# Performance work log

Measured on AMD Instinct MI355X. Metric: run time of the kernel, lower is better.

The kernel has to match this reference:

```python
import jax, jax.numpy as jnp
import numpy as np

HEADS = 8  # init heads


def setup_inputs() -> dict:
    key = jax.random.key(0)
    k1, k2, k3, k4 = jax.random.split(key, 4)
    B, C, L = 32, 512, 32  # batch, dim, lateral_size
    x = jax.random.normal(k1, (B, C, L, L), dtype=jnp.float32)
    # 1x1 conv with no bias == per-pixel matmul; store as [3*dim, dim]
    qkv_w = jax.random.normal(k2, (3 * C, C), dtype=jnp.float32) * (1.0 / np.sqrt(C))
    h_pos = jax.random.normal(k3, (L, 1, C), dtype=jnp.float32) * 0.02
    w_pos = jax.random.normal(k4, (1, L, C), dtype=jnp.float32) * 0.02
    return {"x": x, "qkv_w": qkv_w, "h_pos": h_pos, "w_pos": w_pos}


def reference(x, qkv_w, h_pos, w_pos):
    B, C, H, W = x.shape
    p = HEADS
    d = C // p
    n = H * W
    # QKV 1x1 conv -> [B, 3C, H, W]
    qkv = jnp.einsum('oc,bchw->bohw', qkv_w, x)
    q, k, v = jnp.split(qkv, 3, axis=1)
    # 'b (p d) h w -> b p (h w) d'
    def to_heads(t):
        return t.reshape(B, p, d, H, W).transpose(0, 1, 3, 4, 2).reshape(B, p, n, d)
    q, k, v = to_heads(q), to_heads(k), to_heads(v)
    # relative pos: [H,1,C] + [1,W,C] -> [H,W,C]; 'h w (p d) -> p (h w) d'
    rp = (h_pos + w_pos).reshape(H, W, p, d).transpose(2, 0, 1, 3).reshape(p, n, d)
    # content-position + content-content scores: [B, p, n, n]
    scores = jnp.einsum('bpnd,pmd->bpnm', q, rp) + jnp.einsum('bpnd,bpmd->bpnm', q, k)
    attn = jax.nn.softmax(scores, axis=-1)
    out = jnp.einsum('bpnm,bpmd->bpnd', attn, v)
    # 'b p (h w) d -> b (p d) h w'
    return out.reshape(B, p, H, W, d).transpose(0, 1, 4, 2, 3).reshape(B, C, H, W)
```

## Files before the change

### kernel.cpp

```cpp
#include <hip/hip_runtime.h>
#include <hip/hip_bf16.h>
#include <hip/hip_fp16.h>

#define HEADS 8
#define BB 32
#define CC 512
#define NN 1024
#define DD 64

typedef _Float16 f16;
typedef __attribute__((ext_vector_type(8))) _Float16 f16x8;
typedef __attribute__((ext_vector_type(4))) _Float16 f16x4;
typedef __attribute__((ext_vector_type(2))) __fp16 hf16x2;
typedef __attribute__((ext_vector_type(4))) float f32x4;

__device__ __forceinline__ void gload16(const f16* g, f16* l) {
    __builtin_amdgcn_global_load_lds(
        (const __attribute__((address_space(1))) void*)g,
        (__attribute__((address_space(3))) void*)l, 16, 0, 0);
}

__device__ __forceinline__ void wavefence() {
    asm volatile("s_waitcnt lgkmcnt(0)" ::: "memory");
}

__global__ __launch_bounds__(256) void wconv(
    const float* __restrict__ W, f16* __restrict__ Wh)
{
    const size_t i = ((size_t)blockIdx.x * 256 + threadIdx.x) * 8;
    float4 a = *(const float4*)(W + i);
    float4 b = *(const float4*)(W + i + 4);
    f16x8 h = {(f16)a.x, (f16)a.y, (f16)a.z, (f16)a.w,
               (f16)b.x, (f16)b.y, (f16)b.z, (f16)b.w};
    *(f16x8*)(Wh + i) = h;
}

__global__ __launch_bounds__(256) void prep_x(
    const float* __restrict__ x, f16* __restrict__ xt)
{
    __shared__ f16 T[64][65];
    const int tid = threadIdx.x;
    const int c0 = blockIdx.x * 64;
    const int m0 = blockIdx.y * 64;
    const int b  = blockIdx.z;
    const float* xb = x + (size_t)b * CC * NN;

    const int m_l = tid & 63, c_l = tid >> 6;
    #pragma unroll
    for (int s = 0; s < 16; ++s) {
        const int cr = s * 4 + c_l;
        T[cr][m_l] = (f16)xb[(size_t)(c0 + cr) * NN + m0 + m_l];
    }
    __syncthreads();
    const int m_r = tid >> 2, cq = (tid & 3) * 16;
    f16 buf[16];
    #pragma unroll
    for (int j = 0; j < 16; ++j) buf[j] = T[cq + j][m_r];
    f16* dst = xt + ((size_t)b * NN + m0 + m_r) * CC + c0 + cq;
    *(f16x8*)dst       = *(f16x8*)&buf[0];
    *(f16x8*)(dst + 8) = *(f16x8*)&buf[8];
}

__global__ __launch_bounds__(256) void qkv_mfma(
    const f16*  __restrict__ xt,
    const f16*  __restrict__ Wh,
    const float* __restrict__ h_pos,
    const float* __restrict__ w_pos,
    f16* __restrict__ Qh, f16* __restrict__ Kh, f16* __restrict__ Vt)
{
    __shared__ f16 SM[2 * 128 * 64];
    f16* Xs = SM;
    f16* Ws = SM + 128 * 64;

    const int tid  = threadIdx.x;
    const int wave = tid >> 6, lane = tid & 63;
    const int ln = lane & 15, quad = lane >> 4;

    const unsigned bid  = blockIdx.x;
    const unsigned xcd  = bid & 7;
    const unsigned slot = bid >> 3;
    const unsigned ot   = slot % 12u;
    const unsigned mt   = xcd * 32u + slot / 12u;
    const int o0  = (int)ot * 128;
    const int mg0 = (int)mt * 128;
    const int mw = (wave & 1) * 64, ow = (wave >> 1) * 64;

    f32x4 acc[4][4];
    #pragma unroll
    for (int ia = 0; ia < 4; ++ia)
        #pragma unroll
        for (int ib = 0; ib < 4; ++ib) acc[ia][ib] = (f32x4){0.f, 0.f, 0.f, 0.f};

    const int sr = wave * 32 + (lane >> 3);
    const int sc = (lane & 7) * 8;
    const f16* xg = xt + (size_t)(mg0 + sr) * CC + sc;
    const f16* wg = Wh + (size_t)(o0  + sr) * CC + sc;
    f16* xl = &Xs[(wave * 32) * 64];
    f16* wl = &Ws[(wave * 32) * 64];

    for (int ct = 0; ct < 8; ++ct) {
        const int c0 = ct * 64;
        __syncthreads();
        #pragma unroll
        for (int i = 0; i < 4; ++i) {
            gload16(xg + (size_t)i * 8 * CC + c0, xl + i * 8 * 64);
            gload16(wg + (size_t)i * 8 * CC + c0, wl + i * 8 * 64);
        }
        __syncthreads();
        #pragma unroll
        for (int ks = 0; ks < 2; ++ks) {
            f16x8 a[4], bf[4];
            #pragma unroll
            for (int f = 0; f < 4; ++f) {
                a[f]  = *(const f16x8*)&Xs[(mw + f * 16 + ln) * 64 + ks * 32 + quad * 8];
                bf[f] = *(const f16x8*)&Ws[(ow + f * 16 + ln) * 64 + ks * 32 + quad * 8];
            }
            #pragma unroll
            for (int ia = 0; ia < 4; ++ia)
                #pragma unroll
                for (int ib = 0; ib < 4; ++ib)
                    acc[ia][ib] = __builtin_amdgcn_mfma_f32_16x16x32_f16(
                        a[ia], bf[ib], acc[ia][ib], 0, 0, 0);
        }
    }

    __syncthreads();
    f16* Ep = SM + wave * 4096;

    const int region = o0 >> 9;
    const int ob = o0 + ow;
    const int p  = (ob >> 6) & 7;
    const int b  = mg0 >> 10;
    const int n0 = (mg0 & 1023) + mw;

    if (region < 2) {
        f16* dst = (region == 0) ? Qh : Kh;
        const size_t hb = (size_t)(b * HEADS + p) * NN * DD;
        #pragma unroll
        for (int ph = 0; ph < 2; ++ph) {
            #pragma unroll
            for (int ibl = 0; ibl < 2; ++ibl) {
                const int ib = ph * 2 + ibl;
                const int d  = ib * 16 + ln;
                const int dl = ibl * 16 + ln;
                #pragma unroll
                for (int ia = 0; ia < 4; ++ia) {
                    #pragma unroll
                    for (int r = 0; r < 4; ++r) {
                        const int nl = ia * 16 + quad * 4 + r;
                        float v = acc[ia][ib][r];
                        if (region == 0) {
                            v *= 1.44269504f;
                        } else {
                            const int n = n0 + nl;
                            const int c = p * DD + d;
                            v += h_pos[(n >> 5) * CC + c] + w_pos[(n & 31) * CC + c];
                        }
                        Ep[nl * 34 + dl] = (f16)v;
                    }
                }
            }
            wavefence();
            #pragma unroll
            for (int j = 0; j < 4; ++j) {
                const int nl = (lane >> 2) + 16 * j;
                const int dc = (lane & 3) * 8;
                f16x8 row = *(const f16x8*)&Ep[nl * 34 + dc];
                *(f16x8*)(dst + hb + (size_t)(n0 + nl) * DD + ph * 32 + dc) = row;
            }
            wavefence();
        }
    } else {
        const size_t vb = (size_t)(b * HEADS + p) * DD * NN;
        #pragma unroll
        for (int ph = 0; ph < 2; ++ph) {
            #pragma unroll
            for (int ibl = 0; ibl < 2; ++ibl) {
                const int ib = ph * 2 + ibl;
                const int dl = ibl * 16 + ln;
                #pragma unroll
                for (int ia = 0; ia < 4; ++ia) {
                    const int nl = ia * 16 + quad * 4;
                    f16x4 pk = {(f16)acc[ia][ib][0], (f16)acc[ia][ib][1],
                                (f16)acc[ia][ib][2], (f16)acc[ia][ib][3]};
                    *(f16x4*)&Ep[dl * 68 + nl] = pk;
                }
            }
            wavefence();
            #pragma unroll
            for (int j = 0; j < 4; ++j) {
                const int dl = (lane >> 3) + 8 * j;
                const int nc = (lane & 7) * 8;
                f16x8 row = *(const f16x8*)&Ep[dl * 68 + nc];
                *(f16x8*)(Vt + vb + (size_t)(ph * 32 + dl) * NN + n0 + nc) = row;
            }
            wavefence();
        }
    }
}

#define KST 76

__global__ __launch_bounds__(256) void attn_kernel(
    const f16* __restrict__ Qh, const f16* __restrict__ Kh,
    const f16* __restrict__ Vt, float* __restrict__ out)
{
    __shared__ f16 KS [64 * KST];
    __shared__ f16 VtS[64 * KST];
    __shared__ f16 PS [4][32 * KST];

    const int tid  = threadIdx.x;
    const int wave = tid >> 6;
    const int lane = tid & 63;
    const int ln   = lane & 15;
    const int quad = lane >> 4;

    const unsigned bid  = blockIdx.x;
    const unsigned xcd  = bid & 7;
    const unsigned slot = bid >> 3;
    const int qt = (int)(slot & 7u);
    const unsigned g = xcd * 32u + (slot >> 3);
    const int b = (int)(g >> 3);
    const int p = (int)(g & 7u);
    const size_t hb = (size_t)(b * HEADS + p) * NN * DD;

    const int qbase = qt * 128 + wave * 32;
    f16x8 qf[2][2];
    #pragma unroll
    for (int qa = 0; qa < 2; ++qa)
        #pragma unroll
        for (int ks = 0; ks < 2; ++ks)
            qf[qa][ks] = *(const f16x8*)(
                Qh + hb + (size_t)(qbase + qa * 16 + ln) * DD + ks * 32 + quad * 8);

    f32x4 o[2][4];
    #pragma unroll
    for (int qa = 0; qa < 2; ++qa)
        #pragma unroll
        for (int dt = 0; dt < 4; ++dt) o[qa][dt] = (f32x4){0.f, 0.f, 0.f, 0.f};
    float lrun[2] = {0.f, 0.f};
    float mrun[2] = {-__builtin_inff(), -__builtin_inff()};
    const float THR = 11.5416f;

    const int sr = tid >> 2, sc = (tid & 3) * 16;

    f16x8 kreg0, kreg1, vreg0, vreg1;
    {
        const size_t gk = hb + (size_t)sr * DD + sc;
        kreg0 = *(const f16x8*)(Kh + gk);
        kreg1 = *(const f16x8*)(Kh + gk + 8);
        const size_t gv = hb + (size_t)sr * NN + sc;
        vreg0 = *(const f16x8*)(Vt + gv);
        vreg1 = *(const f16x8*)(Vt + gv + 8);
    }

    f16* Pw = &PS[wave][0];

    for (int kt = 0; kt < 16; ++kt) {
        __syncthreads();
        *(f16x8*)&KS [sr * KST + sc]     = kreg0;
        *(f16x8*)&KS [sr * KST + sc + 8] = kreg1;
        *(f16x8*)&VtS[sr * KST + sc]     = vreg0;
        *(f16x8*)&VtS[sr * KST + sc + 8] = vreg1;
        if (kt < 15) {
            const size_t gk = hb + (size_t)((kt + 1) * 64 + sr) * DD + sc;
            kreg0 = *(const f16x8*)(Kh + gk);
            kreg1 = *(const f16x8*)(Kh + gk + 8);
            const size_t gv = hb + (size_t)sr * NN + (kt + 1) * 64 + sc;
            vreg0 = *(const f16x8*)(Vt + gv);
            vreg1 = *(const f16x8*)(Vt + gv + 8);
        }
        __syncthreads();

        f32x4 s[2][4];
        #pragma unroll
        for (int qa = 0; qa < 2; ++qa)
            #pragma unroll
            for (int nt = 0; nt < 4; ++nt) s[qa][nt] = (f32x4){0.f, 0.f, 0.f, 0.f};
        #pragma unroll
        for (int ks = 0; ks < 2; ++ks) {
            #pragma unroll
            for (int nt = 0; nt < 4; ++nt) {
                f16x8 bk = *(const f16x8*)&KS[(nt * 16 + ln) * KST + ks * 32 + quad * 8];
                s[0][nt] = __builtin_amdgcn_mfma_f32_16x16x32_f16(bk, qf[0][ks], s[0][nt], 0, 0, 0);
                s[1][nt] = __builtin_amdgcn_mfma_f32_16x16x32_f16(bk, qf[1][ks], s[1][nt], 0, 0, 0);
            }
        }

        float mx[2];
        #pragma unroll
        for (int qa = 0; qa < 2; ++qa) {
            float m0 = s[qa][0][0];
            #pragma unroll
            for (int nt = 0; nt < 4; ++nt)
                #pragma unroll
                for (int r = 0; r < 4; ++r) m0 = fmaxf(m0, s[qa][nt][r]);
            m0 = fmaxf(m0, __shfl_xor(m0, 16));
            m0 = fmaxf(m0, __shfl_xor(m0, 32));
            mx[qa] = m0;
        }

        if (__any(mx[0] > mrun[0] + THR || mx[1] > mrun[1] + THR)) {
            #pragma unroll
            for (int qa = 0; qa < 2; ++qa) {
                const float mnew = fmaxf(mrun[qa], mx[qa]);
                const float alpha = __builtin_amdgcn_exp2f(mrun[qa] - mnew);
                mrun[qa] = mnew;
                lrun[qa] *= alpha;
                #pragma unroll
                for (int dt = 0; dt < 4; ++dt) {
                    o[qa][dt][0] *= alpha; o[qa][dt][1] *= alpha;
                    o[qa][dt][2] *= alpha; o[qa][dt][3] *= alpha;
                }
            }
        }

        #pragma unroll
        for (int qa = 0; qa < 2; ++qa) {
            float lsum = 0.f;
            #pragma unroll
            for (int nt = 0; nt < 4; ++nt) {
                const float p0 = __builtin_amdgcn_exp2f(s[qa][nt][0] - mrun[qa]);
                const float p1 = __builtin_amdgcn_exp2f(s[qa][nt][1] - mrun[qa]);
                const float p2 = __builtin_amdgcn_exp2f(s[qa][nt][2] - mrun[qa]);
                const float p3 = __builtin_amdgcn_exp2f(s[qa][nt][3] - mrun[qa]);
                lsum += (p0 + p1) + (p2 + p3);
                hf16x2 lo = __builtin_amdgcn_cvt_pkrtz(p0, p1);
                hf16x2 hi = __builtin_amdgcn_cvt_pkrtz(p2, p3);
                f16x4 pk = {(f16)lo.x, (f16)lo.y, (f16)hi.x, (f16)hi.y};
                *(f16x4*)&Pw[(qa * 16 + ln) * KST + nt * 16 + quad * 4] = pk;
            }
            lsum += __shfl_xor(lsum, 16);
            lsum += __shfl_xor(lsum, 32);
            lrun[qa] += lsum;
        }

        asm volatile("s_waitcnt lgkmcnt(0)" ::: "memory");

        #pragma unroll
        for (int ks = 0; ks < 2; ++ks) {
            f16x8 pa0 = *(const f16x8*)&Pw[(ln)      * KST + ks * 32 + quad * 8];
            f16x8 pa1 = *(const f16x8*)&Pw[(16 + ln) * KST + ks * 32 + quad * 8];
            #pragma unroll
            for (int dt = 0; dt < 4; ++dt) {
                f16x8 vb = *(const f16x8*)&VtS[(dt * 16 + ln) * KST + ks * 32 + quad * 8];
                o[0][dt] = __builtin_amdgcn_mfma_f32_16x16x32_f16(vb, pa0, o[0][dt], 0, 0, 0);
                o[1][dt] = __builtin_amdgcn_mfma_f32_16x16x32_f16(vb, pa1, o[1][dt], 0, 0, 0);
            }
        }
    }

    #pragma unroll
    for (int qa = 0; qa < 2; ++qa) {
        const float inv = 1.0f / lrun[qa];
        const int nq = qbase + qa * 16 + ln;
        #pragma unroll
        for (int dt = 0; dt < 4; ++dt) {
            const int c = p * DD + dt * 16 + quad * 4;
            #pragma unroll
            for (int r = 0; r < 4; ++r)
                out[((size_t)b * CC + c + r) * NN + nq] = o[qa][dt][r] * inv;
        }
    }
}

extern "C" void kernel_launch(void* const* d_in, const int* in_sizes, int n_in,
                              void* d_out, int out_size, void* d_ws, size_t ws_size,
                              hipStream_t stream) {
    const float* x     = (const float*)d_in[0];
    const float* qkv_w = (const float*)d_in[1];
    const float* h_pos = (const float*)d_in[2];
    const float* w_pos = (const float*)d_in[3];
    float* out = (float*)d_out;

    const size_t PT = (size_t)BB * HEADS * NN * DD;
    f16* xt = (f16*)d_ws;
    f16* Qh = xt + PT;
    f16* Kh = Qh + PT;
    f16* Vt = Kh + PT;
    f16* Wh = Vt + PT;

    wconv<<<dim3(3 * CC * CC / (256 * 8)), 256, 0, stream>>>(qkv_w, Wh);
    prep_x<<<dim3(CC / 64, NN / 64, BB), 256, 0, stream>>>(x, xt);
    qkv_mfma<<<dim3(3072), 256, 0, stream>>>(xt, Wh, h_pos, w_pos, Qh, Kh, Vt);
    attn_kernel<<<dim3(2048), 256, 0, stream>>>(Qh, Kh, Vt, out);
}
```

Before: 396.1 us.

## Load K and V fragments directly from global memory, drop LDS staging

The attention kernel no longer stages K and V tiles in shared memory with block-wide barriers. Each wave now reads its MFMA operand fragments for K and V straight from global memory, relying on the L1/L2 caches for reuse across the four waves. This removes two __syncthreads per key tile and the LDS writes, and it lowers LDS usage, which may allow more blocks to be resident. In exchange, global and cache traffic rises fourfold because each wave fetches the same K/V data, and the software prefetch of the next tile is gone, so load latency is exposed.

```diff
diff --git a/kernel.cpp b/kernel.cpp
--- a/kernel.cpp
+++ b/kernel.cpp
@@ -205,9 +205,7 @@
     const f16* __restrict__ Qh, const f16* __restrict__ Kh,
     const f16* __restrict__ Vt, float* __restrict__ out)
 {
-    __shared__ f16 KS [64 * KST];
-    __shared__ f16 VtS[64 * KST];
-    __shared__ f16 PS [4][32 * KST];
+    __shared__ f16 PS[4][32 * KST];
 
     const int tid  = threadIdx.x;
     const int wave = tid >> 6;
@@ -233,6 +231,9 @@
             qf[qa][ks] = *(const f16x8*)(
                 Qh + hb + (size_t)(qbase + qa * 16 + ln) * DD + ks * 32 + quad * 8);
 
+    const f16* Kp = Kh + hb + (size_t)ln * DD + quad * 8;
+    const f16* Vp = Vt + hb + (size_t)ln * NN + quad * 8;
+
     f32x4 o[2][4];
     #pragma unroll
     for (int qa = 0; qa < 2; ++qa)
@@ -242,35 +243,16 @@
     float mrun[2] = {-__builtin_inff(), -__builtin_inff()};
     const float THR = 11.5416f;
 
-    const int sr = tid >> 2, sc = (tid & 3) * 16;
-
-    f16x8 kreg0, kreg1, vreg0, vreg1;
-    {
-        const size_t gk = hb + (size_t)sr * DD + sc;
-        kreg0 = *(const f16x8*)(Kh + gk);
-        kreg1 = *(const f16x8*)(Kh + gk + 8);
-        const size_t gv = hb + (size_t)sr * NN + sc;
-        vreg0 = *(const f16x8*)(Vt + gv);
-        vreg1 = *(const f16x8*)(Vt + gv + 8);
-    }
-
     f16* Pw = &PS[wave][0];
 
     for (int kt = 0; kt < 16; ++kt) {
-        __syncthreads();
-        *(f16x8*)&KS [sr * KST + sc]     = kreg0;
-        *(f16x8*)&KS [sr * KST + sc + 8] = kreg1;
-        *(f16x8*)&VtS[sr * KST + sc]     = vreg0;
-        *(f16x8*)&VtS[sr * KST + sc + 8] = vreg1;
-        if (kt < 15) {
-            const size_t gk = hb + (size_t)((kt + 1) * 64 + sr) * DD + sc;
-            kreg0 = *(const f16x8*)(Kh + gk);
-            kreg1 = *(const f16x8*)(Kh + gk + 8);
-            const size_t gv = hb + (size_t)sr * NN + (kt + 1) * 64 + sc;
-            vreg0 = *(const f16x8*)(Vt + gv);
-            vreg1 = *(const f16x8*)(Vt + gv + 8);
-        }
-        __syncthreads();
+        f16x8 bk[2][4];
+        #pragma unroll
+        for (int ks = 0; ks < 2; ++ks)
+            #pragma unroll
+            for (int nt = 0; nt < 4; ++nt)
+                bk[ks][nt] = *(const f16x8*)(
+                    Kp + (size_t)(kt * 64 + nt * 16) * DD + ks * 32);
 
         f32x4 s[2][4];
         #pragma unroll
@@ -281,9 +263,8 @@
         for (int ks = 0; ks < 2; ++ks) {
             #pragma unroll
             for (int nt = 0; nt < 4; ++nt) {
-                f16x8 bk = *(const f16x8*)&KS[(nt * 16 + ln) * KST + ks * 32 + quad * 8];
-                s[0][nt] = __builtin_amdgcn_mfma_f32_16x16x32_f16(bk, qf[0][ks], s[0][nt], 0, 0, 0);
-                s[1][nt] = __builtin_amdgcn_mfma_f32_16x16x32_f16(bk, qf[1][ks], s[1][nt], 0, 0, 0);
+                s[0][nt] = __builtin_amdgcn_mfma_f32_16x16x32_f16(bk[ks][nt], qf[0][ks], s[0][nt], 0, 0, 0);
+                s[1][nt] = __builtin_amdgcn_mfma_f32_16x16x32_f16(bk[ks][nt], qf[1][ks], s[1][nt], 0, 0, 0);
             }
         }
 
@@ -335,7 +316,7 @@
             lrun[qa] += lsum;
         }
 
-        asm volatile("s_waitcnt lgkmcnt(0)" ::: "memory");
+        wavefence();
 
         #pragma unroll
         for (int ks = 0; ks < 2; ++ks) {
@@ -343,7 +324,8 @@
             f16x8 pa1 = *(const f16x8*)&Pw[(16 + ln) * KST + ks * 32 + quad * 8];
             #pragma unroll
             for (int dt = 0; dt < 4; ++dt) {
-                f16x8 vb = *(const f16x8*)&VtS[(dt * 16 + ln) * KST + ks * 32 + quad * 8];
+                f16x8 vb = *(const f16x8*)(
+                    Vp + (size_t)(dt * 16) * NN + kt * 64 + ks * 32);
                 o[0][dt] = __builtin_amdgcn_mfma_f32_16x16x32_f16(vb, pa0, o[0][dt], 0, 0, 0);
                 o[1][dt] = __builtin_amdgcn_mfma_f32_16x16x32_f16(vb, pa1, o[1][dt], 0, 0, 0);
             }
```

Result: slower. 480.8 us (+21.4%).
